# Optimization experiments

Hardware: AMD Instinct MI355X
Metric: run time of the kernel (lower is better)

The kernel has to match this reference:

```python
import jax, jax.numpy as jnp
import numpy as np
from jax import lax

EXPAND = 64
CHANNELS = 256


def _conv(A, W, padding):
    # NHWC activation, HWIO kernel, stride 1
    return lax.conv_general_dilated(A, W, (1, 1), padding,
                                    dimension_numbers=("NHWC", "HWIO", "NHWC"))


def setup_inputs() -> dict:
    key = jax.random.key(0)
    ks = jax.random.split(key, 7)
    x = jax.random.normal(ks[0], (16, 64, 64, 256), dtype=jnp.float32)
    s = 0.05  # 'random_normal' keras initializer uses stddev=0.05
    w1 = jax.random.normal(ks[1], (1, 1, CHANNELS, EXPAND), dtype=jnp.float32) * s
    b1 = jax.random.normal(ks[2], (1, 1, 1, EXPAND), dtype=jnp.float32) * s
    w2 = jax.random.normal(ks[3], (3, 3, CHANNELS, EXPAND), dtype=jnp.float32) * s
    b2 = jax.random.normal(ks[4], (1, 1, 1, EXPAND), dtype=jnp.float32) * s
    w3 = jax.random.normal(ks[5], (1, 1, CHANNELS, 1), dtype=jnp.float32) * s
    b3 = jax.random.normal(ks[6], (1, 1, 1, 1), dtype=jnp.float32) * s
    return {"x": x, "w1": w1, "b1": b1, "w2": w2, "b2": b2, "w3": w3, "b3": b3}


def reference(x, w1, b1, w2, b2, w3, b3):
    depth_batch = CHANNELS // EXPAND  # gradual-update steps of EXPAND channels

    def step1(A, i):
        Z = _conv(A, w1, "VALID") + b1  # (m,H,W,EXPAND)
        A = lax.dynamic_update_slice(A, Z, (0, 0, 0, i * EXPAND))
        return A, None

    def step2(A, i):
        Z = _conv(A, w2, "SAME") + b2
        A = lax.dynamic_update_slice(A, Z, (0, 0, 0, i * EXPAND))
        return A, None

    def step3(A, i):
        Z = _conv(A, w3, "VALID") + b3  # (m,H,W,1)
        A = lax.dynamic_update_slice(A, Z, (0, 0, 0, i))
        return A, None

    A = x
    A, _ = lax.scan(step1, A, jnp.arange(depth_batch))
    A = jax.nn.relu(A)
    A, _ = lax.scan(step2, A, jnp.arange(depth_batch))
    A = jax.nn.relu(A)
    A, _ = lax.scan(step3, A, jnp.arange(CHANNELS))
    return A + x  # residual shortcut
```

## Files before the change

kernel.cpp:

```cpp
#include <hip/hip_runtime.h>
#include <stdint.h>

typedef unsigned short u16;
typedef unsigned int u32;
typedef __attribute__((ext_vector_type(8))) short short8;
typedef __attribute__((ext_vector_type(4))) short short4v;
typedef __attribute__((ext_vector_type(4))) float f32x4;

#define HW 64
#define CH 256
#define NIMG 16
#define NPIX (NIMG*HW*HW)

static __device__ __forceinline__ u16 f2bf(float f){
  u32 u = __float_as_uint(f);
  u32 r = u + 0x7FFFu + ((u >> 16) & 1u);
  return (u16)(r >> 16);
}
static __device__ __forceinline__ float bf2f(u16 h){
  return __uint_as_float(((u32)h) << 16);
}
static __device__ __forceinline__ u32 relu_pk(u32 w){
  u32 lo = (w & 0x00008000u) ? 0u : (w & 0x0000FFFFu);
  u32 hi = (w & 0x80000000u) ? 0u : (w & 0xFFFF0000u);
  return lo | hi;
}

#define BARRIER_KEEP_VMEM() do { \
  asm volatile("s_waitcnt lgkmcnt(0)" ::: "memory"); \
  __builtin_amdgcn_s_barrier(); \
} while (0)
#define SEG_SYNC() do { \
  asm volatile("s_waitcnt vmcnt(0)" ::: "memory"); \
  asm volatile("s_waitcnt lgkmcnt(0)" ::: "memory"); \
  __builtin_amdgcn_s_barrier(); \
} while (0)

__global__ void k_prep(const float* __restrict__ w1, const float* __restrict__ w2,
                       u16* __restrict__ W1T, u16* __restrict__ W2T){
  int idx = blockIdx.x*256 + threadIdx.x;
  if (idx < 16384){
    int j = idx >> 8, c = idx & 255;
    W1T[idx] = f2bf(w1[c*64 + j]);
  } else {
    int o = idx - 16384;
    int bt  = o / 12288;
    int rem = o - bt*12288;
    int row = rem >> 6;
    int j   = rem & 63;
    int u   = j >> 3, e = j & 7;
    int q = bt / 3, dr = bt - q*3;
    int dc = row >> 6, n = row & 63;
    int cin = q*64 + ((u ^ (row & 7)) << 3) + e;
    int tap = dr*3 + dc;
    W2T[o] = f2bf(w2[(tap*256 + cin)*64 + n]);
  }
}

__global__ __launch_bounds__(256) void k_phase1(const float* __restrict__ x,
    const u16* __restrict__ W1T, const float* __restrict__ b1, u16* __restrict__ B){
  __shared__ u16 At[64*264];
  __shared__ u16 Ws[64*264];
  const int tid = threadIdx.x;
  const long pbase = (long)blockIdx.x * 64;

  #pragma unroll
  for (int it=0; it<16; ++it){
    int idx = it*256 + tid;
    int px = idx >> 6;
    int c4 = (idx & 63) << 2;
    const float4 v = *(const float4*)(x + (pbase + px)*CH + c4);
    short4v s;
    s[0] = (short)f2bf(v.x); s[1] = (short)f2bf(v.y);
    s[2] = (short)f2bf(v.z); s[3] = (short)f2bf(v.w);
    *(short4v*)&At[px*264 + c4] = s;
  }
  #pragma unroll
  for (int it=0; it<8; ++it){
    int idx = it*256 + tid;
    int n = idx >> 5;
    int c8 = (idx & 31) << 3;
    *(uint4*)&Ws[n*264 + c8] = *(const uint4*)&W1T[n*256 + c8];
  }
  __syncthreads();

  const int wave = tid >> 6, lane = tid & 63;
  const int m = lane & 15, quad = lane >> 4;
  const int abase = (wave*16 + m)*264 + quad*8;
  int bbase[4];
  #pragma unroll
  for (int nt=0; nt<4; ++nt) bbase[nt] = (nt*16 + m)*264 + quad*8;
  float b1v[4];
  #pragma unroll
  for (int nt=0; nt<4; ++nt) b1v[nt] = b1[nt*16 + m];

  for (int stepi=0; stepi<4; ++stepi){
    f32x4 acc[4];
    #pragma unroll
    for (int b=0;b<4;++b) acc[b] = 0.f;
    #pragma unroll
    for (int kk=0; kk<8; ++kk){
      const int ko = kk*32;
      short8 af = *(const short8*)&At[abase + ko];
      short8 bf[4];
      #pragma unroll
      for (int nt=0; nt<4; ++nt) bf[nt] = *(const short8*)&Ws[bbase[nt] + ko];
      #pragma unroll
      for (int nt=0; nt<4; ++nt)
        acc[nt] = __builtin_amdgcn_mfma_f32_16x16x32_bf16(af, bf[nt], acc[nt], 0,0,0);
    }
    #pragma unroll
    for (int nt=0; nt<4; ++nt){
      #pragma unroll
      for (int r=0; r<4; ++r){
        int px = wave*16 + quad*4 + r;
        At[px*264 + stepi*64 + nt*16 + m] = f2bf(acc[nt][r] + b1v[nt]);
      }
    }
  }
  __syncthreads();
  #pragma unroll
  for (int it=0; it<16; ++it){
    int idx = it*256 + tid;
    int px = idx >> 6;
    int c4 = (idx & 63) << 2;
    uint2 v = *(const uint2*)&At[px*264 + c4];
    v.x = relu_pk(v.x); v.y = relu_pk(v.y);
    *(uint2*)&B[(pbase + px)*CH + c4] = v;
  }
}

__global__ __launch_bounds__(512) void k_phase2(const u16* __restrict__ B,
    u16* __restrict__ Bout, const u16* __restrict__ W2T, const float* __restrict__ b2,
    const int step){
  __shared__ u16 As[324*76];
  __shared__ u16 Ws[2][192*64];
  const int tid = threadIdx.x;
  const int bid = blockIdx.x;
  const int img = bid >> 4;
  const int R0 = ((bid >> 2) & 3) * 16;
  const int C0 = (bid & 3) * 16;

  const int wave = tid >> 6, lane = tid & 63;
  const int m = lane & 15, quad = lane >> 4;

  uint4 ra[6];

  auto load_as = [&](int q, uint4* r4){
    #pragma unroll
    for (int it=0; it<6; ++it){
      int idx = it*512 + tid;
      uint4 v = make_uint4(0u,0u,0u,0u);
      if (idx < 2592){
        int px = idx >> 3, ck = idx & 7;
        int hr = px / 18, hc = px - hr*18;
        int r = R0 + hr - 1, c = C0 + hc - 1;
        if ((unsigned)r < 64u && (unsigned)c < 64u){
          const u16* src = (q < step) ? Bout : B;
          v = *(const uint4*)&src[((((size_t)img*64)+r)*64 + c)*CH + q*64 + ck*8];
        }
      }
      r4[it] = v;
    }
  };
  auto store_as = [&](const uint4* r4){
    #pragma unroll
    for (int it=0; it<6; ++it){
      int idx = it*512 + tid;
      if (idx < 2592){
        int px = idx >> 3, ck = idx & 7;
        *(uint4*)&As[px*76 + ck*8] = r4[it];
      }
    }
  };
  auto gload_ws = [&](int bt, int buf){
    #pragma unroll
    for (int it=0; it<3; ++it){
      int chunk = wave*3 + it;
      const u16* g = W2T + (size_t)bt*12288 + chunk*512 + lane*8;
      __builtin_amdgcn_global_load_lds(
        (const __attribute__((address_space(1))) void*)g,
        (__attribute__((address_space(3))) void*)&Ws[buf][chunk*512],
        16, 0, 0);
    }
  };

  gload_ws(0, 0);
  load_as(0, ra); store_as(ra);
  __syncthreads();

  f32x4 acc[2][4];
  #pragma unroll
  for (int a=0;a<2;++a){
    #pragma unroll
    for (int b=0;b<4;++b) acc[a][b] = 0.f;
  }

  #pragma unroll
  for (int seg = 0; seg < 12; ++seg){
    const int q  = seg / 3;
    const int dr = seg % 3;

    if (seg <= 10) gload_ws(seg+1, (seg+1)&1);
    if (dr == 1 && q < 3) load_as(q+1, ra);

    const u16* wsb = Ws[seg & 1];
    #pragma unroll
    for (int dc=0; dc<3; ++dc){
      #pragma unroll
      for (int kk=0; kk<2; ++kk){
        short8 af[2], bf[4];
        #pragma unroll
        for (int mt=0; mt<2; ++mt){
          int rt = wave + mt*8;
          af[mt] = *(const short8*)&As[((rt+dr)*18 + m + dc)*76 + kk*32 + quad*8];
        }
        #pragma unroll
        for (int nt=0; nt<4; ++nt){
          int row  = dc*64 + nt*16 + m;
          int unit = (kk*4 + quad) ^ (m & 7);
          bf[nt] = *(const short8*)&wsb[row*64 + unit*8];
        }
        #pragma unroll
        for (int mt=0; mt<2; ++mt){
          #pragma unroll
          for (int nt=0; nt<4; ++nt)
            acc[mt][nt] = __builtin_amdgcn_mfma_f32_16x16x32_bf16(af[mt], bf[nt], acc[mt][nt], 0,0,0);
        }
      }
    }

    if (dr == 2 && q < 3){
      BARRIER_KEEP_VMEM();
      store_as(ra);
    }
    if (seg < 11) SEG_SYNC();
  }

  float b2v[4];
  #pragma unroll
  for (int nt=0; nt<4; ++nt) b2v[nt] = b2[nt*16 + m];
  #pragma unroll
  for (int mt=0; mt<2; ++mt){
    #pragma unroll
    for (int nt=0; nt<4; ++nt){
      #pragma unroll
      for (int r=0; r<4; ++r){
        int row = R0 + wave + mt*8;
        int col = C0 + quad*4 + r;
        size_t gi = ((((size_t)img*64 + row)*64) + col)*CH + step*64 + nt*16 + m;
        Bout[gi] = f2bf(acc[mt][nt][r] + b2v[nt]);
      }
    }
  }
}

__global__ __launch_bounds__(256) void k_phase3(const u16* __restrict__ Bout,
    const float* __restrict__ w3, const float* __restrict__ b3,
    const float* __restrict__ x, float* __restrict__ out){
  __shared__ float w3s[16*17];
  const int tid = threadIdx.x;
  {
    int sseg = tid >> 4, c = tid & 15;
    w3s[sseg*17 + c] = w3[tid];
  }
  const float b3v = b3[0];
  __syncthreads();

  const int g   = blockIdx.x*256 + tid;
  const int px  = g >> 4;
  const int seg = g & 15;
  const size_t cbase = (size_t)px*CH + seg*16;
  const float* wseg = &w3s[seg*17];

  uint4 d[2];
  #pragma unroll
  for (int i=0; i<2; ++i){
    uint4 v = *(const uint4*)&Bout[cbase + i*8];
    v.x = relu_pk(v.x); v.y = relu_pk(v.y); v.z = relu_pk(v.z); v.w = relu_pk(v.w);
    d[i] = v;
  }
  float4 xv[4];
  #pragma unroll
  for (int i=0; i<4; ++i) xv[i] = *(const float4*)&x[cbase + i*4];

  float s0=0.f, s1=0.f;
  #pragma unroll
  for (int i=0; i<2; ++i){
    const u32* p = (const u32*)&d[i];
    #pragma unroll
    for (int k=0; k<4; ++k){
      u32 w = p[k];
      int c = i*8 + k*2;
      s0 += bf2f((u16)(w & 0xFFFF)) * wseg[c];
      s1 += bf2f((u16)(w >> 16))    * wseg[c+1];
    }
  }
  float dot = s0 + s1;
  dot += __shfl_xor(dot, 1, 16);
  dot += __shfl_xor(dot, 2, 16);
  dot += __shfl_xor(dot, 4, 16);
  dot += __shfl_xor(dot, 8, 16);
  const float S0 = b3v + dot;

  float alpha = 1.f, beta = 0.f;
  #pragma unroll
  for (int i=0; i<2; ++i){
    const u32* p = (const u32*)&d[i];
    #pragma unroll
    for (int k=0; k<4; ++k){
      u32 wv = p[k];
      int c = i*8 + k*2;
      float w_a = wseg[c];
      float w_b = wseg[c+1];
      float a_a = bf2f((u16)(wv & 0xFFFF));
      float a_b = bf2f((u16)(wv >> 16));
      beta  = (1.f + w_a)*beta  - w_a*a_a;
      alpha = (1.f + w_a)*alpha;
      beta  = (1.f + w_b)*beta  - w_b*a_b;
      alpha = (1.f + w_b)*alpha;
    }
  }

  float a = alpha, b = beta;
  #pragma unroll
  for (int off=1; off<16; off<<=1){
    float pa = __shfl_up(a, off, 16);
    float pb = __shfl_up(b, off, 16);
    if (seg >= off){ b = a*pb + b; a = a*pa; }
  }
  float ea = __shfl_up(a, 1, 16);
  float eb = __shfl_up(b, 1, 16);
  float Sp = (seg == 0) ? S0 : (ea*S0 + eb);

  #pragma unroll
  for (int i=0; i<2; ++i){
    const u32* p = (const u32*)&d[i];
    float xs[8] = {xv[2*i].x, xv[2*i].y, xv[2*i].z, xv[2*i].w,
                   xv[2*i+1].x, xv[2*i+1].y, xv[2*i+1].z, xv[2*i+1].w};
    float os[8];
    #pragma unroll
    for (int k=0; k<4; ++k){
      u32 wv = p[k];
      int c = i*8 + k*2;
      float w_a = wseg[c];
      float w_b = wseg[c+1];
      float a_a = bf2f((u16)(wv & 0xFFFF));
      float a_b = bf2f((u16)(wv >> 16));
      os[k*2]   = Sp + xs[k*2];
      Sp = (1.f + w_a)*Sp - w_a*a_a;
      os[k*2+1] = Sp + xs[k*2+1];
      Sp = (1.f + w_b)*Sp - w_b*a_b;
    }
    float4 o0, o1;
    o0.x=os[0]; o0.y=os[1]; o0.z=os[2]; o0.w=os[3];
    o1.x=os[4]; o1.y=os[5]; o1.z=os[6]; o1.w=os[7];
    *(float4*)&out[cbase + i*8]     = o0;
    *(float4*)&out[cbase + i*8 + 4] = o1;
  }
}

extern "C" void kernel_launch(void* const* d_in, const int* in_sizes, int n_in,
                              void* d_out, int out_size, void* d_ws, size_t ws_size,
                              hipStream_t stream){
  const float* x  = (const float*)d_in[0];
  const float* w1 = (const float*)d_in[1];
  const float* b1 = (const float*)d_in[2];
  const float* w2 = (const float*)d_in[3];
  const float* b2 = (const float*)d_in[4];
  const float* w3 = (const float*)d_in[5];
  const float* b3 = (const float*)d_in[6];
  float* out = (float*)d_out;

  u16* B    = (u16*)d_ws;
  u16* Bout = B    + (size_t)NPIX*CH;
  u16* W1T  = Bout + (size_t)NPIX*CH;
  u16* W2T  = W1T  + 16384;

  hipLaunchKernelGGL(k_prep,   dim3(640),  dim3(256), 0, stream, w1, w2, W1T, W2T);
  hipLaunchKernelGGL(k_phase1, dim3(1024), dim3(256), 0, stream, x, W1T, b1, B);
  for (int s = 0; s < 4; ++s)
    hipLaunchKernelGGL(k_phase2, dim3(256), dim3(512), 0, stream, B, Bout, W2T, b2, s);
  hipLaunchKernelGGL(k_phase3, dim3(4096), dim3(256), 0, stream, Bout, w3, b3, x, out);
}
```

Baseline: 248.2 us.

## Make later 3x3 conv steps incremental updates from the changed channel block

Conv is linear, and each gradual-update step changes only one 64-channel block of the input. So steps 1–3 now compute the previous step's output plus a 3x3 conv of only the delta block (new minus original), using a 64-input-channel slice of the weights. The first pass runs the full conv as before and stores an fp32 running sum S and a bf16 delta buffer. The new k_phase2d kernel then does a quarter of the MFMA work per step and ping-pongs delta buffers. The cost is extra global traffic for the fp32 S and the delta buffers, and added bf16 rounding error that builds up across steps.

```diff
diff --git a/kernel.cpp b/kernel.cpp
--- a/kernel.cpp
+++ b/kernel.cpp
@@ -132,7 +132,7 @@
 
 __global__ __launch_bounds__(512) void k_phase2(const u16* __restrict__ B,
     u16* __restrict__ Bout, const u16* __restrict__ W2T, const float* __restrict__ b2,
-    const int step){
+    float* __restrict__ S, u16* __restrict__ D0){
   __shared__ u16 As[324*76];
   __shared__ u16 Ws[2][192*64];
   const int tid = threadIdx.x;
@@ -155,10 +155,8 @@
         int px = idx >> 3, ck = idx & 7;
         int hr = px / 18, hc = px - hr*18;
         int r = R0 + hr - 1, c = C0 + hc - 1;
-        if ((unsigned)r < 64u && (unsigned)c < 64u){
-          const u16* src = (q < step) ? Bout : B;
-          v = *(const uint4*)&src[((((size_t)img*64)+r)*64 + c)*CH + q*64 + ck*8];
-        }
+        if ((unsigned)r < 64u && (unsigned)c < 64u)
+          v = *(const uint4*)&B[((((size_t)img*64)+r)*64 + c)*CH + q*64 + ck*8];
       }
       r4[it] = v;
     }
@@ -248,8 +246,109 @@
       for (int r=0; r<4; ++r){
         int row = R0 + wave + mt*8;
         int col = C0 + quad*4 + r;
-        size_t gi = ((((size_t)img*64 + row)*64) + col)*CH + step*64 + nt*16 + m;
-        Bout[gi] = f2bf(acc[mt][nt][r] + b2v[nt]);
+        int ch  = nt*16 + m;
+        size_t pix = ((size_t)img*64 + row)*64 + col;
+        float z = acc[mt][nt][r] + b2v[nt];
+        S[pix*64 + ch] = z;
+        Bout[pix*CH + ch] = f2bf(z);
+        float bq = bf2f(B[pix*CH + ch]);
+        D0[pix*64 + ch] = f2bf(z - bq);
+      }
+    }
+  }
+}
+
+__global__ __launch_bounds__(512) void k_phase2d(const u16* __restrict__ Din,
+    u16* __restrict__ Dout, float* __restrict__ S, u16* __restrict__ Bout,
+    const u16* __restrict__ B, const u16* __restrict__ W2T, const int step){
+  __shared__ u16 Ds[324*76];
+  __shared__ u16 Wq[576*64];
+  const int tid = threadIdx.x;
+  const int bid = blockIdx.x;
+  const int img = bid >> 4;
+  const int R0 = ((bid >> 2) & 3) * 16;
+  const int C0 = (bid & 3) * 16;
+
+  const int wave = tid >> 6, lane = tid & 63;
+  const int m = lane & 15, quad = lane >> 4;
+
+  const u16* wbase = W2T + (size_t)(step-1)*36864;
+  #pragma unroll
+  for (int it=0; it<9; ++it){
+    int chunk = wave*9 + it;
+    const u16* g = wbase + chunk*512 + lane*8;
+    __builtin_amdgcn_global_load_lds(
+      (const __attribute__((address_space(1))) void*)g,
+      (__attribute__((address_space(3))) void*)&Wq[chunk*512],
+      16, 0, 0);
+  }
+  #pragma unroll
+  for (int it=0; it<6; ++it){
+    int idx = it*512 + tid;
+    if (idx < 2592){
+      int px = idx >> 3, ck = idx & 7;
+      int hr = px / 18, hc = px - hr*18;
+      int r = R0 + hr - 1, c = C0 + hc - 1;
+      uint4 v = make_uint4(0u,0u,0u,0u);
+      if ((unsigned)r < 64u && (unsigned)c < 64u)
+        v = *(const uint4*)&Din[((((size_t)img*64)+r)*64 + c)*64 + ck*8];
+      *(uint4*)&Ds[px*76 + ck*8] = v;
+    }
+  }
+  __syncthreads();
+
+  f32x4 acc[2][4];
+  #pragma unroll
+  for (int a=0;a<2;++a){
+    #pragma unroll
+    for (int b=0;b<4;++b) acc[a][b] = 0.f;
+  }
+
+  #pragma unroll
+  for (int dr=0; dr<3; ++dr){
+    #pragma unroll
+    for (int dc=0; dc<3; ++dc){
+      #pragma unroll
+      for (int kk=0; kk<2; ++kk){
+        short8 af[2], bf[4];
+        #pragma unroll
+        for (int mt=0; mt<2; ++mt){
+          int rt = wave + mt*8;
+          af[mt] = *(const short8*)&Ds[((rt+dr)*18 + m + dc)*76 + kk*32 + quad*8];
+        }
+        #pragma unroll
+        for (int nt=0; nt<4; ++nt){
+          int row  = dr*192 + dc*64 + nt*16 + m;
+          int unit = (kk*4 + quad) ^ (m & 7);
+          bf[nt] = *(const short8*)&Wq[row*64 + unit*8];
+        }
+        #pragma unroll
+        for (int mt=0; mt<2; ++mt){
+          #pragma unroll
+          for (int nt=0; nt<4; ++nt)
+            acc[mt][nt] = __builtin_amdgcn_mfma_f32_16x16x32_bf16(af[mt], bf[nt], acc[mt][nt], 0,0,0);
+        }
+      }
+    }
+  }
+
+  #pragma unroll
+  for (int mt=0; mt<2; ++mt){
+    #pragma unroll
+    for (int nt=0; nt<4; ++nt){
+      #pragma unroll
+      for (int r=0; r<4; ++r){
+        int row = R0 + wave + mt*8;
+        int col = C0 + quad*4 + r;
+        int ch  = nt*16 + m;
+        size_t pix = ((size_t)img*64 + row)*64 + col;
+        float s = S[pix*64 + ch] + acc[mt][nt][r];
+        S[pix*64 + ch] = s;
+        Bout[pix*CH + step*64 + ch] = f2bf(s);
+        if (step < 3){
+          float bq = bf2f(B[pix*CH + step*64 + ch]);
+          Dout[pix*64 + ch] = f2bf(s - bq);
+        }
       }
     }
   }
@@ -376,10 +475,15 @@
   u16* Bout = B    + (size_t)NPIX*CH;
   u16* W1T  = Bout + (size_t)NPIX*CH;
   u16* W2T  = W1T  + 16384;
+  float* S  = (float*)(W2T + 147456);
+  u16* D0   = (u16*)(S + (size_t)NPIX*64);
+  u16* D1   = D0 + (size_t)NPIX*64;
 
   hipLaunchKernelGGL(k_prep,   dim3(640),  dim3(256), 0, stream, w1, w2, W1T, W2T);
   hipLaunchKernelGGL(k_phase1, dim3(1024), dim3(256), 0, stream, x, W1T, b1, B);
-  for (int s = 0; s < 4; ++s)
-    hipLaunchKernelGGL(k_phase2, dim3(256), dim3(512), 0, stream, B, Bout, W2T, b2, s);
+  hipLaunchKernelGGL(k_phase2, dim3(256),  dim3(512), 0, stream, B, Bout, W2T, b2, S, D0);
+  hipLaunchKernelGGL(k_phase2d, dim3(256), dim3(512), 0, stream, D0, D1, S, Bout, B, W2T, 1);
+  hipLaunchKernelGGL(k_phase2d, dim3(256), dim3(512), 0, stream, D1, D0, S, Bout, B, W2T, 2);
+  hipLaunchKernelGGL(k_phase2d, dim3(256), dim3(512), 0, stream, D0, D1, S, Bout, B, W2T, 3);
   hipLaunchKernelGGL(k_phase3, dim3(4096), dim3(256), 0, stream, Bout, w3, b3, x, out);
 }
```

Result: slower. 278.9 us (+12.4%).

## Split K across wave groups in phase2 conv with LDS reduction

Applied to the files above, without the earlier changes.

Phase2's 3x3 conv now splits the 64-channel K dimension between two groups of four waves. Each wave covers four row tiles instead of two and does one kk slice instead of two, so each B fragment feeds four MFMAs instead of two and LDS reads of W per MFMA drop. The partial sums are reduced through LDS scratch in two halves before the biased bf16 store. This costs more accumulator registers, extra barriers and LDS traffic in the epilogue, and leaves only half the waves doing the final stores.

```diff
diff --git a/kernel.cpp b/kernel.cpp
--- a/kernel.cpp
+++ b/kernel.cpp
@@ -143,6 +143,7 @@
 
   const int wave = tid >> 6, lane = tid & 63;
   const int m = lane & 15, quad = lane >> 4;
+  const int g = wave >> 2, wr = wave & 3;
 
   uint4 ra[6];
 
@@ -177,9 +178,9 @@
     #pragma unroll
     for (int it=0; it<3; ++it){
       int chunk = wave*3 + it;
-      const u16* g = W2T + (size_t)bt*12288 + chunk*512 + lane*8;
+      const u16* g2 = W2T + (size_t)bt*12288 + chunk*512 + lane*8;
       __builtin_amdgcn_global_load_lds(
-        (const __attribute__((address_space(1))) void*)g,
+        (const __attribute__((address_space(1))) void*)g2,
         (__attribute__((address_space(3))) void*)&Ws[buf][chunk*512],
         16, 0, 0);
     }
@@ -189,9 +190,9 @@
   load_as(0, ra); store_as(ra);
   __syncthreads();
 
-  f32x4 acc[2][4];
-  #pragma unroll
-  for (int a=0;a<2;++a){
+  f32x4 acc[4][4];
+  #pragma unroll
+  for (int a=0;a<4;++a){
     #pragma unroll
     for (int b=0;b<4;++b) acc[a][b] = 0.f;
   }
@@ -207,26 +208,23 @@
     const u16* wsb = Ws[seg & 1];
     #pragma unroll
     for (int dc=0; dc<3; ++dc){
-      #pragma unroll
-      for (int kk=0; kk<2; ++kk){
-        short8 af[2], bf[4];
+      short8 af[4], bf[4];
+      #pragma unroll
+      for (int mt=0; mt<4; ++mt){
+        int rt = wr + mt*4;
+        af[mt] = *(const short8*)&As[((rt+dr)*18 + m + dc)*76 + g*32 + quad*8];
+      }
+      #pragma unroll
+      for (int nt=0; nt<4; ++nt){
+        int row  = dc*64 + nt*16 + m;
+        int unit = (g*4 + quad) ^ (m & 7);
+        bf[nt] = *(const short8*)&wsb[row*64 + unit*8];
+      }
+      #pragma unroll
+      for (int mt=0; mt<4; ++mt){
         #pragma unroll
-        for (int mt=0; mt<2; ++mt){
-          int rt = wave + mt*8;
-          af[mt] = *(const short8*)&As[((rt+dr)*18 + m + dc)*76 + kk*32 + quad*8];
-        }
-        #pragma unroll
-        for (int nt=0; nt<4; ++nt){
-          int row  = dc*64 + nt*16 + m;
-          int unit = (kk*4 + quad) ^ (m & 7);
-          bf[nt] = *(const short8*)&wsb[row*64 + unit*8];
-        }
-        #pragma unroll
-        for (int mt=0; mt<2; ++mt){
-          #pragma unroll
-          for (int nt=0; nt<4; ++nt)
-            acc[mt][nt] = __builtin_amdgcn_mfma_f32_16x16x32_bf16(af[mt], bf[nt], acc[mt][nt], 0,0,0);
-        }
+        for (int nt=0; nt<4; ++nt)
+          acc[mt][nt] = __builtin_amdgcn_mfma_f32_16x16x32_bf16(af[mt], bf[nt], acc[mt][nt], 0,0,0);
       }
     }
 
@@ -237,19 +235,43 @@
     if (seg < 11) SEG_SYNC();
   }
 
+  float* scr = (float*)As;
   float b2v[4];
   #pragma unroll
   for (int nt=0; nt<4; ++nt) b2v[nt] = b2[nt*16 + m];
-  #pragma unroll
-  for (int mt=0; mt<2; ++mt){
-    #pragma unroll
-    for (int nt=0; nt<4; ++nt){
-      #pragma unroll
-      for (int r=0; r<4; ++r){
-        int row = R0 + wave + mt*8;
-        int col = C0 + quad*4 + r;
-        size_t gi = ((((size_t)img*64 + row)*64) + col)*CH + step*64 + nt*16 + m;
-        Bout[gi] = f2bf(acc[mt][nt][r] + b2v[nt]);
+
+  #pragma unroll
+  for (int half=0; half<2; ++half){
+    BARRIER_KEEP_VMEM();
+    if (g == 1){
+      #pragma unroll
+      for (int mh=0; mh<2; ++mh){
+        int mt = half*2 + mh;
+        #pragma unroll
+        for (int nt=0; nt<4; ++nt){
+          #pragma unroll
+          for (int r=0; r<4; ++r)
+            scr[(((wr*2 + mh)*4 + nt)*4 + r)*64 + lane] = acc[mt][nt][r];
+        }
+      }
+    }
+    BARRIER_KEEP_VMEM();
+    if (g == 0){
+      #pragma unroll
+      for (int mh=0; mh<2; ++mh){
+        int mt = half*2 + mh;
+        #pragma unroll
+        for (int nt=0; nt<4; ++nt){
+          #pragma unroll
+          for (int r=0; r<4; ++r){
+            float v = acc[mt][nt][r]
+                    + scr[(((wr*2 + mh)*4 + nt)*4 + r)*64 + lane] + b2v[nt];
+            int row = R0 + wr + mt*4;
+            int col = C0 + quad*4 + r;
+            size_t gi = ((((size_t)img*64 + row)*64) + col)*CH + step*64 + nt*16 + m;
+            Bout[gi] = f2bf(v);
+          }
+        }
       }
     }
   }
```

New measurement: 250.4 us. Within noise of the previous version (+0.9%).

## Load full per-quarter weight slab into LDS, cutting phase2 barriers to four

Applied to the files above, without the earlier changes.

Phase 2 previously streamed weights into a double buffer in twelve segments, with a barrier after each. It now loads all nine taps of a 64-channel input quarter (576x64 bf16) into LDS at once, so only one barrier is needed per quarter. The goal is to remove most of the synchronisation overhead. In exchange, weight loads are no longer overlapped with compute within a quarter, and LDS use grows, which may lower occupancy.

```diff
diff --git a/kernel.cpp b/kernel.cpp
--- a/kernel.cpp
+++ b/kernel.cpp
@@ -134,7 +134,7 @@
     u16* __restrict__ Bout, const u16* __restrict__ W2T, const float* __restrict__ b2,
     const int step){
   __shared__ u16 As[324*76];
-  __shared__ u16 Ws[2][192*64];
+  __shared__ u16 Wq[576*64];
   const int tid = threadIdx.x;
   const int bid = blockIdx.x;
   const int img = bid >> 4;
@@ -173,19 +173,20 @@
       }
     }
   };
-  auto gload_ws = [&](int bt, int buf){
-    #pragma unroll
-    for (int it=0; it<3; ++it){
-      int chunk = wave*3 + it;
-      const u16* g = W2T + (size_t)bt*12288 + chunk*512 + lane*8;
+  auto gload_wq = [&](int q){
+    const u16* wbase = W2T + (size_t)q*36864;
+    #pragma unroll
+    for (int it=0; it<9; ++it){
+      int chunk = wave*9 + it;
+      const u16* g = wbase + chunk*512 + lane*8;
       __builtin_amdgcn_global_load_lds(
         (const __attribute__((address_space(1))) void*)g,
-        (__attribute__((address_space(3))) void*)&Ws[buf][chunk*512],
+        (__attribute__((address_space(3))) void*)&Wq[chunk*512],
         16, 0, 0);
     }
   };
 
-  gload_ws(0, 0);
+  gload_wq(0);
   load_as(0, ra); store_as(ra);
   __syncthreads();
 
@@ -196,45 +197,43 @@
     for (int b=0;b<4;++b) acc[a][b] = 0.f;
   }
 
-  #pragma unroll
-  for (int seg = 0; seg < 12; ++seg){
-    const int q  = seg / 3;
-    const int dr = seg % 3;
-
-    if (seg <= 10) gload_ws(seg+1, (seg+1)&1);
-    if (dr == 1 && q < 3) load_as(q+1, ra);
-
-    const u16* wsb = Ws[seg & 1];
-    #pragma unroll
-    for (int dc=0; dc<3; ++dc){
-      #pragma unroll
-      for (int kk=0; kk<2; ++kk){
-        short8 af[2], bf[4];
+  for (int q = 0; q < 4; ++q){
+    if (q < 3) load_as(q+1, ra);
+
+    #pragma unroll
+    for (int dr=0; dr<3; ++dr){
+      #pragma unroll
+      for (int dc=0; dc<3; ++dc){
         #pragma unroll
-        for (int mt=0; mt<2; ++mt){
-          int rt = wave + mt*8;
-          af[mt] = *(const short8*)&As[((rt+dr)*18 + m + dc)*76 + kk*32 + quad*8];
+        for (int kk=0; kk<2; ++kk){
+          short8 af[2], bf[4];
+          #pragma unroll
+          for (int mt=0; mt<2; ++mt){
+            int rt = wave + mt*8;
+            af[mt] = *(const short8*)&As[((rt+dr)*18 + m + dc)*76 + kk*32 + quad*8];
+          }
+          #pragma unroll
+          for (int nt=0; nt<4; ++nt){
+            int row  = dr*192 + dc*64 + nt*16 + m;
+            int unit = (kk*4 + quad) ^ (m & 7);
+            bf[nt] = *(const short8*)&Wq[row*64 + unit*8];
+          }
+          #pragma unroll
+          for (int mt=0; mt<2; ++mt){
+            #pragma unroll
+            for (int nt=0; nt<4; ++nt)
+              acc[mt][nt] = __builtin_amdgcn_mfma_f32_16x16x32_bf16(af[mt], bf[nt], acc[mt][nt], 0,0,0);
+          }
         }
-        #pragma unroll
-        for (int nt=0; nt<4; ++nt){
-          int row  = dc*64 + nt*16 + m;
-          int unit = (kk*4 + quad) ^ (m & 7);
-          bf[nt] = *(const short8*)&wsb[row*64 + unit*8];
-        }
-        #pragma unroll
-        for (int mt=0; mt<2; ++mt){
-          #pragma unroll
-          for (int nt=0; nt<4; ++nt)
-            acc[mt][nt] = __builtin_amdgcn_mfma_f32_16x16x32_bf16(af[mt], bf[nt], acc[mt][nt], 0,0,0);
-        }
-      }
-    }
-
-    if (dr == 2 && q < 3){
+      }
+    }
+
+    if (q < 3){
       BARRIER_KEEP_VMEM();
+      gload_wq(q+1);
       store_as(ra);
-    }
-    if (seg < 11) SEG_SYNC();
+      SEG_SYNC();
+    }
   }
 
   float b2v[4];
```

Measured after the change: 252.5 us. About the same (+1.7%).
